# Kernel tuning notes

Measured on AMD Instinct MI355X. Metric: run time of the kernel, lower is better.

Reference implementation:

```python
import jax, jax.numpy as jnp
import numpy as np

N_NODES = 50000
N_EDGES = 800000
IN_CH = 128
OUT_CH = 64


def setup_inputs() -> dict:
    key = jax.random.key(0)
    ks = jax.random.split(key, 8)
    cat = IN_CH + OUT_CH
    scale = 1.0 / np.sqrt(cat)
    return {
        "x": jax.random.normal(ks[0], (N_NODES, IN_CH), dtype=jnp.float32),
        "edge_index": jax.random.randint(ks[1], (2, N_EDGES), 0, N_NODES, dtype=jnp.int64),
        "edge_weight": jax.random.uniform(ks[2], (N_EDGES,), dtype=jnp.float32),
        "hidden_state": jax.random.normal(ks[3], (N_NODES, OUT_CH), dtype=jnp.float32),
        "W_z": jax.random.normal(ks[4], (cat, OUT_CH), dtype=jnp.float32) * scale,
        "b_z": jnp.zeros((OUT_CH,), dtype=jnp.float32),
        "W_r": jax.random.normal(ks[5], (cat, OUT_CH), dtype=jnp.float32) * scale,
        "b_r": jnp.zeros((OUT_CH,), dtype=jnp.float32),
        "W_h": jax.random.normal(ks[6], (cat, OUT_CH), dtype=jnp.float32) * scale,
        "b_h": jnp.zeros((OUT_CH,), dtype=jnp.float32),
    }


def _gcn_norm(row, col, w, num_nodes):
    # PyG GCNConv normalization with self-loops (fill_value=1):
    # norm_e = deg[row]^-1/2 * w_e * deg[col]^-1/2 over loop-augmented edges
    loops = jnp.arange(num_nodes, dtype=row.dtype)
    row = jnp.concatenate([row, loops])
    col = jnp.concatenate([col, loops])
    w = jnp.concatenate([w, jnp.ones((num_nodes,), dtype=w.dtype)])
    deg = jax.ops.segment_sum(w, col, num_segments=num_nodes)
    dinv = jnp.where(deg > 0, jax.lax.rsqrt(deg), 0.0)
    norm = dinv[row] * w * dinv[col]
    return row, col, norm


def _gcn_conv(x_cat, W, b, row, col, norm, num_nodes):
    h = x_cat @ W                                   # (N, out)
    msg = h[row] * norm[:, None]                    # (E+N, out) gather + scale
    out = jax.ops.segment_sum(msg, col, num_segments=num_nodes)
    return out + b


def reference(x, edge_index, edge_weight, hidden_state,
              W_z, b_z, W_r, b_r, W_h, b_h):
    n = x.shape[0]
    row, col, norm = _gcn_norm(edge_index[0], edge_index[1], edge_weight, n)
    xh = jnp.concatenate([x, hidden_state], axis=1)
    z = jax.nn.sigmoid(_gcn_conv(xh, W_z, b_z, row, col, norm, n))
    r = jax.nn.sigmoid(_gcn_conv(xh, W_r, b_r, row, col, norm, n))
    xrh = jnp.concatenate([x, r * hidden_state], axis=1)
    h_cand = jnp.tanh(_gcn_conv(xrh, W_h, b_h, row, col, norm, n))
    return z * hidden_state + (1.0 - z) * h_cand
```

## Files before the change

### kernel.cpp

```cpp
#include <hip/hip_runtime.h>
#include <hip/hip_bf16.h>
#include <cstdint>
#include <cstddef>

#define IN_CH   128
#define OUT_CH  64
#define CAT_CH  192

typedef short bf16x8 __attribute__((ext_vector_type(8)));
typedef float f32x4  __attribute__((ext_vector_type(4)));
typedef float f32x2  __attribute__((ext_vector_type(2)));
typedef unsigned long long u64;
typedef unsigned int u32;

__device__ __forceinline__ float sigmoidf_(float x) { return 1.f / (1.f + __expf(-x)); }

__device__ __forceinline__ unsigned short f2bf(float f) {
    u32 u = __float_as_uint(f);
    u32 r = (u + 0x7fffu + ((u >> 16) & 1u)) >> 16;
    return (unsigned short)r;
}
__device__ __forceinline__ float bflo(u32 v) { return __uint_as_float(v << 16); }
__device__ __forceinline__ float bfhi(u32 v) { return __uint_as_float(v & 0xffff0000u); }
__device__ __forceinline__ float bf1(unsigned short v) { return __uint_as_float((u32)v << 16); }

__device__ __forceinline__ unsigned char f2e4m3(float f) {
    u32 p = __builtin_amdgcn_cvt_pk_fp8_f32(f, f, 0, false);
    return (unsigned char)p;
}
__device__ __forceinline__ f32x2 e4m3x2_to_f(u32 two) {
    return __builtin_amdgcn_cvt_pk_f32_fp8(two, false);
}

__global__ void detect_kernel(const unsigned int* __restrict__ ei, int* __restrict__ flag) {
    unsigned int v = ei[(threadIdx.x << 1) + 1];
    unsigned long long b = __ballot(v != 0u);
    if (threadIdx.x == 0) *flag = (b != 0ull) ? 1 : 0;
}

__device__ __forceinline__ int load_col(const void* ei, int i, int E, int f) {
    return f ? ((const int*)ei)[E + i] : (int)((const long long*)ei)[E + i];
}
__device__ __forceinline__ int load_row(const void* ei, int i, int E, int f) {
    return f ? ((const int*)ei)[i] : (int)((const long long*)ei)[i];
}

__global__ void hist2_kernel(const void* __restrict__ ei, const float* __restrict__ w,
                             u64* __restrict__ packed, u32* __restrict__ rank,
                             const int* __restrict__ flag, int E) {
    int i0 = (blockIdx.x * blockDim.x + threadIdx.x) * 4;
    if (i0 >= E) return;
    int f = *flag;
    u32 rk[4];
#pragma unroll
    for (int k = 0; k < 4; k++) {
        int i = i0 + k;
        if (i < E) {
            int c = load_col(ei, i, E, f);
            u32 wq = __float2uint_rn(w[i] * 1048576.0f);
            u64 old = atomicAdd(&packed[c], (1ull << 32) | (u64)wq);
            rk[k] = (u32)(old >> 32);
        }
    }
#pragma unroll
    for (int k = 0; k < 4; k++)
        if (i0 + k < E) rank[i0 + k] = rk[k];
}

__global__ __launch_bounds__(256) void scan1_kernel(const u64* __restrict__ packed,
                                                    float* __restrict__ dinv,
                                                    int* __restrict__ starts,
                                                    int* __restrict__ bsum, int n) {
    __shared__ int s[256];
    int i = blockIdx.x * 256 + threadIdx.x;
    int v = 0;
    if (i < n) {
        u64 p = packed[i];
        float wsum = (float)(u32)(p & 0xffffffffull) * (1.0f / 1048576.0f);
        dinv[i] = rsqrtf(1.0f + wsum);
        v = (int)(p >> 32);
    }
    s[threadIdx.x] = v;
    __syncthreads();
#pragma unroll
    for (int d = 1; d < 256; d <<= 1) {
        int t = (threadIdx.x >= d) ? s[threadIdx.x - d] : 0;
        __syncthreads();
        s[threadIdx.x] += t;
        __syncthreads();
    }
    if (i < n) starts[i] = s[threadIdx.x] - v;
    if (threadIdx.x == 255) bsum[blockIdx.x] = s[255];
}

__global__ __launch_bounds__(256) void scan2_kernel(int* __restrict__ bsum, int nb) {
    __shared__ int s[256];
    int t = threadIdx.x;
    int v = (t < nb) ? bsum[t] : 0;
    s[t] = v;
    __syncthreads();
#pragma unroll
    for (int d = 1; d < 256; d <<= 1) {
        int u = (t >= d) ? s[t - d] : 0;
        __syncthreads();
        s[t] += u;
        __syncthreads();
    }
    if (t < nb) bsum[t] = s[t] - v;
}

__global__ void scan3_kernel(int* __restrict__ starts, const int* __restrict__ boff,
                             int n, int E) {
    int i = blockIdx.x * blockDim.x + threadIdx.x;
    if (i == 0) starts[n] = E;
    if (i < n) starts[i] += boff[blockIdx.x];
}

__global__ void scatter2_kernel(const void* __restrict__ ei, const float* __restrict__ w,
                                const float* __restrict__ dinv, const int* __restrict__ starts,
                                const u32* __restrict__ rank, u64* __restrict__ pairs,
                                const int* __restrict__ flag, int E) {
    int i0 = (blockIdx.x * blockDim.x + threadIdx.x) * 4;
    if (i0 >= E) return;
    int f = *flag;
    int r[4], c[4];
#pragma unroll
    for (int k = 0; k < 4; k++) {
        int i = i0 + k;
        if (i < E) { r[k] = load_row(ei, i, E, f); c[k] = load_col(ei, i, E, f); }
    }
#pragma unroll
    for (int k = 0; k < 4; k++) {
        int i = i0 + k;
        if (i < E) {
            float nm = dinv[r[k]] * w[i] * dinv[c[k]];
            int pos = starts[c[k]] + (int)rank[i];
            pairs[pos] = ((u64)__float_as_uint(nm) << 32) | (u32)r[k];
        }
    }
}

__global__ void cvt_kernel(const float* __restrict__ x, const float* __restrict__ hidden,
                           unsigned short* __restrict__ xb, unsigned short* __restrict__ hb,
                           int nx, int nh) {
    int i4 = (blockIdx.x * blockDim.x + threadIdx.x) * 4;
    if (i4 < nx) {
        float4 v = *(const float4*)&x[i4];
        ushort4 o = { f2bf(v.x), f2bf(v.y), f2bf(v.z), f2bf(v.w) };
        *(ushort4*)&xb[i4] = o;
    } else {
        int j = i4 - nx;
        if (j < nh) {
            float4 v = *(const float4*)&hidden[j];
            ushort4 o = { f2bf(v.x), f2bf(v.y), f2bf(v.z), f2bf(v.w) };
            *(ushort4*)&hb[j] = o;
        }
    }
}

__global__ void packW_kernel(const float* __restrict__ Wz, const float* __restrict__ Wr,
                             const float* __restrict__ Wh,
                             unsigned short* __restrict__ Bzrt, unsigned short* __restrict__ Wht) {
    int i = blockIdx.x * blockDim.x + threadIdx.x;
    if (i >= 192 * CAT_CH) return;
    int col = i / CAT_CH, k = i % CAT_CH;
    if (col < 128) {
        float v = (col < 64) ? Wz[k * 64 + col] : Wr[k * 64 + (col - 64)];
        Bzrt[col * CAT_CH + k] = f2bf(v);
    } else {
        Wht[(col - 128) * CAT_CH + k] = f2bf(Wh[k * 64 + (col - 128)]);
    }
}

template <int TN, bool FP8OUT>
__global__ __launch_bounds__(256) void gemm_bf16_kernel(
    const unsigned short* __restrict__ A0, int a0w,
    const unsigned short* __restrict__ A1, int a1w,
    const unsigned short* __restrict__ Bt,
    void* __restrict__ Cout, int nrows)
{
    __shared__ unsigned short As[128][48];
    __shared__ unsigned short Bs[TN][200];

    const int t = threadIdx.x, lane = t & 63, wave = t >> 6;
    const int rowBase = blockIdx.x * 128;

    for (int idx = t * 8; idx < TN * CAT_CH; idx += 256 * 8) {
        int col = idx / CAT_CH, k = idx % CAT_CH;
        *(int4*)&Bs[col][k] = *(const int4*)&Bt[idx];
    }

    f32x4 acc[2][TN / 16];
#pragma unroll
    for (int rf = 0; rf < 2; rf++)
#pragma unroll
        for (int cf = 0; cf < TN / 16; cf++) acc[rf][cf] = (f32x4){0.f, 0.f, 0.f, 0.f};

    const int srow = t >> 1, half = t & 1;
    int arow = rowBase + srow;
    if (arow >= nrows) arow = nrows - 1;

    for (int k0 = 0; k0 < CAT_CH; k0 += 32) {
        __syncthreads();
        {
            const unsigned short* src = (k0 < a0w)
                ? A0 + (size_t)arow * a0w + k0
                : A1 + (size_t)arow * a1w + (k0 - a0w);
            *(int4*)&As[srow][half * 16] = *(const int4*)(src + half * 16);
            *(int4*)&As[srow][half * 16 + 8] = *(const int4*)(src + half * 16 + 8);
        }
        __syncthreads();

        const int rbase = wave * 32;
        const int koff = (lane >> 4) * 8;
        bf16x8 a0 = *(const bf16x8*)&As[rbase + (lane & 15)][koff];
        bf16x8 a1 = *(const bf16x8*)&As[rbase + 16 + (lane & 15)][koff];
#pragma unroll
        for (int cf = 0; cf < TN / 16; cf++) {
            bf16x8 b = *(const bf16x8*)&Bs[cf * 16 + (lane & 15)][k0 + koff];
            acc[0][cf] = __builtin_amdgcn_mfma_f32_16x16x32_bf16(a0, b, acc[0][cf], 0, 0, 0);
            acc[1][cf] = __builtin_amdgcn_mfma_f32_16x16x32_bf16(a1, b, acc[1][cf], 0, 0, 0);
        }
    }

#pragma unroll
    for (int rf = 0; rf < 2; rf++)
#pragma unroll
        for (int cf = 0; cf < TN / 16; cf++) {
            int row0 = rowBase + wave * 32 + rf * 16 + (lane >> 4) * 4;
            int col  = cf * 16 + (lane & 15);
#pragma unroll
            for (int r = 0; r < 4; r++) {
                int row = row0 + r;
                if (row < nrows) {
                    if (FP8OUT)
                        ((unsigned char*)Cout)[(size_t)row * TN + col] = f2e4m3(acc[rf][cf][r]);
                    else
                        ((unsigned short*)Cout)[(size_t)row * TN + col] = f2bf(acc[rf][cf][r]);
                }
            }
        }
}

__global__ __launch_bounds__(256) void spmm_zr_kernel(
    const unsigned char* __restrict__ H8, const u64* __restrict__ pairs,
    const int* __restrict__ starts, const float* __restrict__ dinv,
    const float* __restrict__ hidden, const float* __restrict__ bz,
    const float* __restrict__ br, float* __restrict__ Z,
    unsigned short* __restrict__ RHb, int N)
{
    int node = (blockIdx.x * 256 + threadIdx.x) >> 6;
    if (node >= N) return;
    int lane = threadIdx.x & 63;
    int s = starts[node], e = starts[node + 1];
    float d = dinv[node], d2 = d * d;
    const int ch = lane * 2;

    u32 self = *(const unsigned short*)&H8[(size_t)node * 128 + ch];
    f32x2 sv = e4m3x2_to_f(self);
    float ax = sv.x * d2, ay = sv.y * d2;

    for (int j = s; j < e; j += 8) {
        u32 hv[8]; float nm[8];
#pragma unroll
        for (int k = 0; k < 8; k++) {
            int jj = j + k;
            u64 p = pairs[(jj < e) ? jj : (e - 1)];
            nm[k] = (jj < e) ? __uint_as_float((u32)(p >> 32)) : 0.f;
            hv[k] = *(const unsigned short*)&H8[(size_t)(u32)p * 128 + ch];
        }
#pragma unroll
        for (int k = 0; k < 8; k++) {
            f32x2 hf = e4m3x2_to_f(hv[k]);
            ax = fmaf(hf.x, nm[k], ax);
            ay = fmaf(hf.y, nm[k], ay);
        }
    }

    if (lane < 32) {
        int c = ch;
        float2 o = { sigmoidf_(ax + bz[c]), sigmoidf_(ay + bz[c + 1]) };
        *(float2*)&Z[(size_t)node * 64 + c] = o;
    } else {
        int c = ch - 64;
        const float* hid = hidden + (size_t)node * 64 + c;
        float rh0 = sigmoidf_(ax + br[c])     * hid[0];
        float rh1 = sigmoidf_(ay + br[c + 1]) * hid[1];
        u32 packed = (u32)f2bf(rh0) | ((u32)f2bf(rh1) << 16);
        *(u32*)&RHb[(size_t)node * 64 + c] = packed;
    }
}

__global__ __launch_bounds__(256) void spmm_h_kernel(
    const unsigned short* __restrict__ H, const u64* __restrict__ pairs,
    const int* __restrict__ starts, const float* __restrict__ dinv,
    const float* __restrict__ hidden, const float* __restrict__ bh,
    const float* __restrict__ Z, float* __restrict__ out, int N)
{
    int node = (blockIdx.x * 256 + threadIdx.x) >> 6;
    if (node >= N) return;
    int lane = threadIdx.x & 63;
    int s = starts[node], e = starts[node + 1];
    float d = dinv[node], d2 = d * d;

    float acc = bf1(H[(size_t)node * 64 + lane]) * d2;

    for (int j = s; j < e; j += 8) {
        unsigned short hv[8]; float nm[8];
#pragma unroll
        for (int k = 0; k < 8; k++) {
            int jj = j + k;
            u64 p = pairs[(jj < e) ? jj : (e - 1)];
            nm[k] = (jj < e) ? __uint_as_float((u32)(p >> 32)) : 0.f;
            hv[k] = H[(size_t)(u32)p * 64 + lane];
        }
#pragma unroll
        for (int k = 0; k < 8; k++)
            acc = fmaf(bf1(hv[k]), nm[k], acc);
    }

    size_t idx = (size_t)node * 64 + lane;
    float hc = tanhf(acc + bh[lane]);
    float z  = Z[idx];
    out[idx] = z * hidden[idx] + (1.f - z) * hc;
}

extern "C" void kernel_launch(void* const* d_in, const int* in_sizes, int n_in,
                              void* d_out, int out_size, void* d_ws, size_t ws_size,
                              hipStream_t stream) {
    const float* x      = (const float*)d_in[0];
    const void*  eidx   = d_in[1];
    const float* ew     = (const float*)d_in[2];
    const float* hidden = (const float*)d_in[3];
    const float* Wz     = (const float*)d_in[4];
    const float* bz     = (const float*)d_in[5];
    const float* Wr     = (const float*)d_in[6];
    const float* br     = (const float*)d_in[7];
    const float* Wh     = (const float*)d_in[8];
    const float* bh     = (const float*)d_in[9];
    float* out = (float*)d_out;

    const int E = in_sizes[2];
    const int N = in_sizes[3] / OUT_CH;

    char* base = (char*)d_ws;
    size_t off = 0;
    auto carve = [&](size_t bytes) -> char* {
        char* p = base + off;
        off = (off + bytes + 255) & ~(size_t)255;
        return p;
    };
    u64*   packed = (u64*)  carve((size_t)N * 8);
    u32*   rank   = (u32*)  carve((size_t)E * 4);
    float* dinv   = (float*)carve((size_t)N * 4);
    int*   starts = (int*)  carve((size_t)(N + 1) * 4);
    int*   bsum   = (int*)  carve(256 * 4);
    u64*   pairs  = (u64*)  carve((size_t)E * 8);
    unsigned short* xb   = (unsigned short*)carve((size_t)N * 128 * 2);
    unsigned short* hb   = (unsigned short*)carve((size_t)N * 64 * 2);
    unsigned char*  Hzr8 = (unsigned char*)carve((size_t)N * 128);
    unsigned short* RHb  = (unsigned short*)carve((size_t)N * 64 * 2);
    unsigned short* Hhb  = (unsigned short*)carve((size_t)N * 64 * 2);
    float* Z = (float*)carve((size_t)N * 64 * 4);
    unsigned short* Bzrt = (unsigned short*)carve((size_t)128 * CAT_CH * 2);
    unsigned short* Wht  = (unsigned short*)carve((size_t)64 * CAT_CH * 2);
    int* flag = (int*)carve(4);
    if (off > ws_size) return;

    const int B256 = 256;
    const int gE4 = (E + 1023) / 1024;
    const int gN = (N + B256 - 1) / B256;
    const int gM = (N + 127) / 128;
    const int gW = (N + 3) / 4;

    hipLaunchKernelGGL(detect_kernel, dim3(1), dim3(64), 0, stream,
                       (const unsigned int*)eidx, flag);

    hipMemsetAsync(packed, 0, (size_t)N * 8, stream);
    hipLaunchKernelGGL(hist2_kernel, dim3(gE4), dim3(B256), 0, stream,
                       eidx, ew, packed, rank, flag, E);

    hipLaunchKernelGGL(scan1_kernel, dim3(gN), dim3(B256), 0, stream,
                       packed, dinv, starts, bsum, N);
    hipLaunchKernelGGL(scan2_kernel, dim3(1), dim3(B256), 0, stream, bsum, gN);
    hipLaunchKernelGGL(scan3_kernel, dim3(gN), dim3(B256), 0, stream, starts, bsum, N, E);

    hipLaunchKernelGGL(scatter2_kernel, dim3(gE4), dim3(B256), 0, stream,
                       eidx, ew, dinv, starts, rank, pairs, flag, E);

    hipLaunchKernelGGL(cvt_kernel, dim3((N * CAT_CH / 4 + 255) / 256), dim3(B256), 0, stream,
                       x, hidden, xb, hb, N * 128, N * 64);
    hipLaunchKernelGGL(packW_kernel, dim3((192 * CAT_CH + 255) / 256), dim3(B256), 0, stream,
                       Wz, Wr, Wh, Bzrt, Wht);

    hipLaunchKernelGGL((gemm_bf16_kernel<128, true>), dim3(gM), dim3(B256), 0, stream,
                       xb, 128, hb, 64, Bzrt, (void*)Hzr8, N);

    hipLaunchKernelGGL(spmm_zr_kernel, dim3(gW), dim3(B256), 0, stream,
                       Hzr8, pairs, starts, dinv, hidden, bz, br, Z, RHb, N);

    hipLaunchKernelGGL((gemm_bf16_kernel<64, false>), dim3(gM), dim3(B256), 0, stream,
                       xb, 128, RHb, 64, Wht, (void*)Hhb, N);

    hipLaunchKernelGGL(spmm_h_kernel, dim3(gW), dim3(B256), 0, stream,
                       Hhb, pairs, starts, dinv, hidden, bh, Z, out, N);
}
```

Before: 200.0 us.

## Split each wavefront into two half-waves processing alternate edges in SpMM

```diff
diff --git a/kernel.cpp b/kernel.cpp
--- a/kernel.cpp
+++ b/kernel.cpp
@@ -22,14 +22,14 @@
 }
 __device__ __forceinline__ float bflo(u32 v) { return __uint_as_float(v << 16); }
 __device__ __forceinline__ float bfhi(u32 v) { return __uint_as_float(v & 0xffff0000u); }
-__device__ __forceinline__ float bf1(unsigned short v) { return __uint_as_float((u32)v << 16); }
 
 __device__ __forceinline__ unsigned char f2e4m3(float f) {
     u32 p = __builtin_amdgcn_cvt_pk_fp8_f32(f, f, 0, false);
     return (unsigned char)p;
 }
-__device__ __forceinline__ f32x2 e4m3x2_to_f(u32 two) {
-    return __builtin_amdgcn_cvt_pk_f32_fp8(two, false);
+template <bool HI>
+__device__ __forceinline__ f32x2 fp8pk(u32 v) {
+    return __builtin_amdgcn_cvt_pk_f32_fp8((int)v, HI);
 }
 
 __global__ void detect_kernel(const unsigned int* __restrict__ ei, int* __restrict__ flag) {
@@ -135,7 +135,7 @@
         if (i < E) {
             float nm = dinv[r[k]] * w[i] * dinv[c[k]];
             int pos = starts[c[k]] + (int)rank[i];
-            pairs[pos] = ((u64)__float_as_uint(nm) << 32) | (u32)r[k];
+            pairs[pos] = ((u64)__float_as_uint(nm) << 32) | (u32)(r[k] << 7);
         }
     }
 }
@@ -251,43 +251,75 @@
 {
     int node = (blockIdx.x * 256 + threadIdx.x) >> 6;
     if (node >= N) return;
-    int lane = threadIdx.x & 63;
+    const int lane = threadIdx.x & 63;
+    const int sub = lane & 31, half = lane >> 5;
     int s = starts[node], e = starts[node + 1];
     float d = dinv[node], d2 = d * d;
-    const int ch = lane * 2;
-
-    u32 self = *(const unsigned short*)&H8[(size_t)node * 128 + ch];
-    f32x2 sv = e4m3x2_to_f(self);
-    float ax = sv.x * d2, ay = sv.y * d2;
-
-    for (int j = s; j < e; j += 8) {
+
+    float a0 = 0.f, a1 = 0.f, a2 = 0.f, a3 = 0.f;
+    if (half == 0) {
+        u32 sv = *(const u32*)&H8[(size_t)node * 128 + sub * 4];
+        f32x2 s01 = fp8pk<false>(sv), s23 = fp8pk<true>(sv);
+        a0 = s01.x * d2; a1 = s01.y * d2; a2 = s23.x * d2; a3 = s23.y * d2;
+    }
+
+    int j = s;
+    int full = s + ((e - s) & ~15);
+    for (; j < full; j += 16) {
         u32 hv[8]; float nm[8];
 #pragma unroll
         for (int k = 0; k < 8; k++) {
-            int jj = j + k;
+            u64 p = pairs[j + k * 2 + half];
+            nm[k] = __uint_as_float((u32)(p >> 32));
+            hv[k] = *(const u32*)&H8[(size_t)(u32)p + sub * 4];
+        }
+#pragma unroll
+        for (int k = 0; k < 8; k++) {
+            f32x2 h01 = fp8pk<false>(hv[k]), h23 = fp8pk<true>(hv[k]);
+            a0 = fmaf(h01.x, nm[k], a0); a1 = fmaf(h01.y, nm[k], a1);
+            a2 = fmaf(h23.x, nm[k], a2); a3 = fmaf(h23.y, nm[k], a3);
+        }
+    }
+    if (j < e) {
+        u32 hv[8]; float nm[8];
+#pragma unroll
+        for (int k = 0; k < 8; k++) {
+            int jj = j + k * 2 + half;
             u64 p = pairs[(jj < e) ? jj : (e - 1)];
             nm[k] = (jj < e) ? __uint_as_float((u32)(p >> 32)) : 0.f;
-            hv[k] = *(const unsigned short*)&H8[(size_t)(u32)p * 128 + ch];
-        }
-#pragma unroll
-        for (int k = 0; k < 8; k++) {
-            f32x2 hf = e4m3x2_to_f(hv[k]);
-            ax = fmaf(hf.x, nm[k], ax);
-            ay = fmaf(hf.y, nm[k], ay);
-        }
-    }
-
-    if (lane < 32) {
-        int c = ch;
-        float2 o = { sigmoidf_(ax + bz[c]), sigmoidf_(ay + bz[c + 1]) };
-        *(float2*)&Z[(size_t)node * 64 + c] = o;
-    } else {
-        int c = ch - 64;
-        const float* hid = hidden + (size_t)node * 64 + c;
-        float rh0 = sigmoidf_(ax + br[c])     * hid[0];
-        float rh1 = sigmoidf_(ay + br[c + 1]) * hid[1];
-        u32 packed = (u32)f2bf(rh0) | ((u32)f2bf(rh1) << 16);
-        *(u32*)&RHb[(size_t)node * 64 + c] = packed;
+            hv[k] = *(const u32*)&H8[(size_t)(u32)p + sub * 4];
+        }
+#pragma unroll
+        for (int k = 0; k < 8; k++) {
+            f32x2 h01 = fp8pk<false>(hv[k]), h23 = fp8pk<true>(hv[k]);
+            a0 = fmaf(h01.x, nm[k], a0); a1 = fmaf(h01.y, nm[k], a1);
+            a2 = fmaf(h23.x, nm[k], a2); a3 = fmaf(h23.y, nm[k], a3);
+        }
+    }
+
+    a0 += __shfl_xor(a0, 32, 64);
+    a1 += __shfl_xor(a1, 32, 64);
+    a2 += __shfl_xor(a2, 32, 64);
+    a3 += __shfl_xor(a3, 32, 64);
+
+    if (half == 0) {
+        if (sub < 16) {
+            int c = sub * 4;
+            float4 b4 = *(const float4*)&bz[c];
+            float4 o = { sigmoidf_(a0 + b4.x), sigmoidf_(a1 + b4.y),
+                         sigmoidf_(a2 + b4.z), sigmoidf_(a3 + b4.w) };
+            *(float4*)&Z[(size_t)node * 64 + c] = o;
+        } else {
+            int c = (sub - 16) * 4;
+            float4 b4 = *(const float4*)&br[c];
+            float4 hid = *(const float4*)&hidden[(size_t)node * 64 + c];
+            float r0 = sigmoidf_(a0 + b4.x) * hid.x;
+            float r1 = sigmoidf_(a1 + b4.y) * hid.y;
+            float r2 = sigmoidf_(a2 + b4.z) * hid.z;
+            float r3 = sigmoidf_(a3 + b4.w) * hid.w;
+            ushort4 o = { f2bf(r0), f2bf(r1), f2bf(r2), f2bf(r3) };
+            *(ushort4*)&RHb[(size_t)node * 64 + c] = o;
+        }
     }
 }
 
@@ -299,30 +331,64 @@
 {
     int node = (blockIdx.x * 256 + threadIdx.x) >> 6;
     if (node >= N) return;
-    int lane = threadIdx.x & 63;
+    const int lane = threadIdx.x & 63;
+    const int sub = lane & 31, half = lane >> 5;
+    const unsigned char* Hb = (const unsigned char*)H;
     int s = starts[node], e = starts[node + 1];
     float d = dinv[node], d2 = d * d;
 
-    float acc = bf1(H[(size_t)node * 64 + lane]) * d2;
-
-    for (int j = s; j < e; j += 8) {
-        unsigned short hv[8]; float nm[8];
-#pragma unroll
-        for (int k = 0; k < 8; k++) {
-            int jj = j + k;
+    float ax = 0.f, ay = 0.f;
+    if (half == 0) {
+        u32 sv = *(const u32*)&Hb[(size_t)node * 128 + sub * 4];
+        ax = bflo(sv) * d2; ay = bfhi(sv) * d2;
+    }
+
+    int j = s;
+    int full = s + ((e - s) & ~15);
+    for (; j < full; j += 16) {
+        u32 hv[8]; float nm[8];
+#pragma unroll
+        for (int k = 0; k < 8; k++) {
+            u64 p = pairs[j + k * 2 + half];
+            nm[k] = __uint_as_float((u32)(p >> 32));
+            hv[k] = *(const u32*)&Hb[(size_t)(u32)p + sub * 4];
+        }
+#pragma unroll
+        for (int k = 0; k < 8; k++) {
+            ax = fmaf(bflo(hv[k]), nm[k], ax);
+            ay = fmaf(bfhi(hv[k]), nm[k], ay);
+        }
+    }
+    if (j < e) {
+        u32 hv[8]; float nm[8];
+#pragma unroll
+        for (int k = 0; k < 8; k++) {
+            int jj = j + k * 2 + half;
             u64 p = pairs[(jj < e) ? jj : (e - 1)];
             nm[k] = (jj < e) ? __uint_as_float((u32)(p >> 32)) : 0.f;
-            hv[k] = H[(size_t)(u32)p * 64 + lane];
-        }
-#pragma unroll
-        for (int k = 0; k < 8; k++)
-            acc = fmaf(bf1(hv[k]), nm[k], acc);
-    }
-
-    size_t idx = (size_t)node * 64 + lane;
-    float hc = tanhf(acc + bh[lane]);
-    float z  = Z[idx];
-    out[idx] = z * hidden[idx] + (1.f - z) * hc;
+            hv[k] = *(const u32*)&Hb[(size_t)(u32)p + sub * 4];
+        }
+#pragma unroll
+        for (int k = 0; k < 8; k++) {
+            ax = fmaf(bflo(hv[k]), nm[k], ax);
+            ay = fmaf(bfhi(hv[k]), nm[k], ay);
+        }
+    }
+
+    ax += __shfl_xor(ax, 32, 64);
+    ay += __shfl_xor(ay, 32, 64);
+
+    if (half == 0) {
+        int c = sub * 2;
+        size_t idx = (size_t)node * 64 + c;
+        float2 hid = *(const float2*)&hidden[idx];
+        float2 z   = *(const float2*)&Z[idx];
+        float hc0 = tanhf(ax + bh[c]);
+        float hc1 = tanhf(ay + bh[c + 1]);
+        float2 o = { z.x * hid.x + (1.f - z.x) * hc0,
+                     z.y * hid.y + (1.f - z.y) * hc1 };
+        *(float2*)&out[idx] = o;
+    }
 }
 
 extern "C" void kernel_launch(void* const* d_in, const int* in_sizes, int n_in,
@@ -376,7 +442,7 @@
     hipLaunchKernelGGL(detect_kernel, dim3(1), dim3(64), 0, stream,
                        (const unsigned int*)eidx, flag);
 
-    hipMemsetAsync(packed, 0, (size_t)N * 8, stream);
+    (void)hipMemsetAsync(packed, 0, (size_t)N * 8, stream);
     hipLaunchKernelGGL(hist2_kernel, dim3(gE4), dim3(B256), 0, stream,
                        eidx, ew, packed, rank, flag, E);
 
```

Measured after the change: 178.7 us. -10.6%, faster.
